# Performance work log

Hardware: AMD Instinct MI355X
Metric: run time of the kernel (lower is better)

Reference implementation:

```python
import jax
import jax.numpy as jnp
from jax import lax
import numpy as np

INPUT_DIM = 784
HIDDEN_DIM = 1024
BATCH = 256
N_BINS = 10


def setup_inputs() -> dict:
    key = jax.random.key(0)
    k1, k2, k3, k4, k5 = jax.random.split(key, 5)
    # kaiming-normal-ish init scales (faithful in spirit; exact values irrelevant for math)
    W = jax.random.normal(k1, (HIDDEN_DIM, INPUT_DIM), dtype=jnp.float32) * np.sqrt(2.0 / INPUT_DIM)
    c = jnp.zeros((HIDDEN_DIM, 1), dtype=jnp.float32)
    V = jax.random.normal(k2, (INPUT_DIM, HIDDEN_DIM, N_BINS), dtype=jnp.float32) * np.sqrt(2.0 / N_BINS)
    b = jnp.zeros((INPUT_DIM, N_BINS), dtype=jnp.float32)
    x = jax.random.randint(k3, (BATCH, INPUT_DIM), 0, N_BINS, dtype=jnp.int32)
    return {"x": x, "W": W, "c": c, "V": V, "b": b}


def reference(x, W, c, V, b):
    # x: [B, D] int pixel bins; W: [H, D]; c: [H, 1]; V: [D, H, 10]; b: [D, 10]
    B = x.shape[0]
    xf = x.astype(jnp.float32)  # [B, D]
    a0 = jnp.broadcast_to(c[:, 0][None, :], (B, W.shape[0]))  # [B, H]

    def step(a, inp):
        Vi, bi, Wi, xi = inp  # Vi:[H,10], bi:[10], Wi:[H], xi:[B]
        h = jax.nn.sigmoid(a)                       # [B, H]
        p = jax.nn.softmax(h @ Vi + bi, axis=1)     # [B, 10]
        a = a + xi[:, None] * Wi[None, :]           # rank-1 update, matches x_i @ W[:,i].T
        return a, p

    _, p_seq = lax.scan(step, a0, (V, b, W.T, xf.T))  # p_seq: [D, B, 10]
    p_hat = jnp.transpose(p_seq, (1, 2, 0))            # [B, 10, D] == torch.stack(p_hat, dim=2)
    return p_hat
```

## Files before the change

### kernel.cpp

```cpp
#include <hip/hip_runtime.h>
#include <stdint.h>

#define D_DIM 784
#define H_DIM 1024
#define B_DIM 256
#define NBIN  10
#define G_CH  16
#define T_CH  49
#define P_CH  8
#define T_PS  98
#define BT    16
#define LOG2E 1.4426950408889634f

#define VPREP_BLKS D_DIM
#define WPREP_BLKS 208

typedef _Float16 half8_t  __attribute__((ext_vector_type(8)));
typedef __fp16   fp16x2_t __attribute__((ext_vector_type(2)));
typedef float    float4_t __attribute__((ext_vector_type(4)));

__global__ void k_prep(const float* __restrict__ W, const float* __restrict__ V,
                       _Float16* __restrict__ Wt2h, _Float16* __restrict__ VB) {
    __shared__ __align__(16) float smem[5120];
    int tid = threadIdx.x;
    int bx  = blockIdx.x;

    if (bx < VPREP_BLKS) {
        int i = bx;
        const float4* src = (const float4*)(V + (size_t)i * H_DIM * NBIN);
        uint4* dst = (uint4*)VB + (size_t)i * 2048;
        #pragma unroll
        for (int p = 0; p < 2; ++p) {
            if (p) __syncthreads();
            #pragma unroll
            for (int qv = 0; qv < 5; ++qv) {
                float4 v = src[p * 1280 + qv * 256 + tid];
                *((float4*)&smem[(qv * 256 + tid) * 4]) = v;
            }
            __syncthreads();
            #pragma unroll
            for (int qv = 0; qv < 4; ++qv) {
                int pair = p * 1024 + qv * 256 + tid;
                int kk = pair >> 6, ll = pair & 63;
                int n = ll & 15, hb = kk * 32 + ((ll >> 4) & 3) * 8;
                union { _Float16 hh[8]; uint4 u; } o;
                #pragma unroll
                for (int jj = 0; jj < 8; ++jj)
                    o.hh[jj] = (_Float16)((n < NBIN) ? smem[(hb + jj) * NBIN + n - p * 5120] : 0.0f);
                dst[pair] = o.u;
            }
        }
    } else {
        int qw = bx - VPREP_BLKS;
        int j0 = (qw % 13) * 64, h0 = (qw / 13) * 64;
        float (*t)[65] = (float(*)[65])smem;
        int tj = tid & 63, tr = tid >> 6;
        int j = j0 + tj;
        #pragma unroll
        for (int r = 0; r < 16; ++r) {
            int hh = tr * 16 + r;
            t[hh][tj] = (j < D_DIM) ? W[(size_t)(h0 + hh) * D_DIM + j] : 0.0f;
        }
        __syncthreads();
        #pragma unroll
        for (int r = 0; r < 16; ++r) {
            int jj = tr * 16 + r;
            int jo = j0 + jj;
            if (jo < D_DIM) Wt2h[(size_t)jo * H_DIM + h0 + tj] = (_Float16)(t[tj][jj] * LOG2E);
        }
    }
}

__global__ __launch_bounds__(256)
void k_pscan(const _Float16* __restrict__ Wt2h, const int* __restrict__ x,
             const float* __restrict__ c, _Float16* __restrict__ PA) {
    int b   = blockIdx.x;
    int hg  = blockIdx.y;
    int tid = threadIdx.x;
    int hcol = hg * 256 + tid;
    int h0   = hcol * 2;

    __shared__ float xs[D_DIM];
    if (tid < D_DIM / 4) {
        int4 xi = ((const int4*)(x + (size_t)b * D_DIM))[tid];
        *((float4*)&xs[tid * 4]) =
            make_float4((float)xi.x, (float)xi.y, (float)xi.z, (float)xi.w);
    }
    float acc0 = c[h0] * LOG2E, acc1 = c[h0 + 1] * LOG2E;
    __syncthreads();

    const uint* wp  = (const uint*)Wt2h;
    uint*       pau = (uint*)PA;

    uint wvA[8], wvB[8];
    auto ldrow = [&](int t, uint (&wv)[8]) {
        #pragma unroll
        for (int r = 0; r < 8; ++r)
            wv[r] = wp[(size_t)(t * 8 + r) * 512 + hcol];
    };
    auto emit = [&](int t) {
        union { _Float16 hh[2]; uint u; } uu;
        uu.hh[0] = (_Float16)acc0; uu.hh[1] = (_Float16)acc1;
        pau[((size_t)t * B_DIM + b) * 512 + hcol] = uu.u;
    };
    auto fmas = [&](int t, const uint (&wv)[8]) {
        #pragma unroll
        for (int r = 0; r < 8; ++r) {
            union { uint u; _Float16 hh[2]; } uu; uu.u = wv[r];
            float xf = xs[t * 8 + r];
            acc0 += xf * (float)uu.hh[0];
            acc1 += xf * (float)uu.hh[1];
        }
    };

    ldrow(0, wvA);
    for (int t = 0; t < T_PS; t += 2) {
        ldrow(t + 1, wvB);
        emit(t);     fmas(t, wvA);
        if (t + 2 < T_PS) ldrow(t + 2, wvA);
        emit(t + 1); fmas(t + 1, wvB);
    }
}

__global__ __launch_bounds__(512, 2)
void k_main(const _Float16* __restrict__ VB, const _Float16* __restrict__ Wt2h,
            const _Float16* __restrict__ PA, const int* __restrict__ x,
            const float* __restrict__ bias, float* __restrict__ out) {
    int bid = blockIdx.x;
    int lb  = (bid & 7) * 98 + (bid >> 3);
    int tc  = lb >> 4;
    int bt  = lb & 15;
    int tid = threadIdx.x;
    int g   = tid >> 8;
    int w   = (tid >> 6) & 3;
    int l   = tid & 63;
    int bl  = l & 15;
    int kg  = l >> 4;
    int bg  = bt * BT + bl;
    int ib  = tc * G_CH;
    int i0  = ib + g * P_CH;

    __shared__ float red[2][4][64][17];
    __shared__ float bs[G_CH][16];

    {
        if (tid < 256) {
            int ii = tid >> 4, n = tid & 15;
            bs[ii][n] = (n < NBIN) ? bias[(size_t)(ib + ii) * NBIN + n] : 0.0f;
        }
    }

    float a[8][8];
    {
        int ct = tc * 2 + g;
        const _Float16* src = PA + ((size_t)ct * B_DIM + bg) * H_DIM + w * 256 + kg * 8;
        #pragma unroll
        for (int m = 0; m < 8; ++m) {
            half8_t av = *((const half8_t*)(src + m * 32));
            #pragma unroll
            for (int j = 0; j < 8; ++j) a[m][j] = (float)av[j];
        }
    }

    const int4* xp = (const int4*)(x + (size_t)bg * D_DIM + i0);

    const uint4* vp = (const uint4*)VB + ((size_t)i0 * 32 + w * 8) * 64 + l;
    uint4 vbuf[4];
    vbuf[0] = vp[0];
    vbuf[1] = vp[64];
    const uint4* vpr = vp + 128;

    const _Float16* whp = Wt2h + (size_t)i0 * H_DIM + w * 256 + kg * 8;
    half8_t whbuf[2];
    whbuf[0] = *((const half8_t*)whp);
    whbuf[1] = *((const half8_t*)(whp + 32));
    const _Float16* whr = whp + 64;

    float4_t acc = {0.f, 0.f, 0.f, 0.f};

    auto softmax_store = [&](int q) {
        float p4[4];
        #pragma unroll
        for (int qq = 0; qq < 4; ++qq) {
            float tot = red[g][0][l][qq * 4 + w] + red[g][1][l][qq * 4 + w]
                      + red[g][2][l][qq * 4 + w] + red[g][3][l][qq * 4 + w];
            float v = (bl < NBIN) ? tot + bs[g * P_CH + q * 4 + qq][bl] : -3.0e38f;
            float vm = v;
            vm = fmaxf(vm, __shfl_xor(vm, 1));
            vm = fmaxf(vm, __shfl_xor(vm, 2));
            vm = fmaxf(vm, __shfl_xor(vm, 4));
            vm = fmaxf(vm, __shfl_xor(vm, 8));
            float e = __builtin_amdgcn_exp2f((v - vm) * LOG2E);
            float ss = e;
            ss += __shfl_xor(ss, 1); ss += __shfl_xor(ss, 2);
            ss += __shfl_xor(ss, 4); ss += __shfl_xor(ss, 8);
            p4[qq] = e * __builtin_amdgcn_rcpf(ss);
        }
        if (bl < NBIN) {
            int b = bt * BT + kg * 4 + w;
            size_t base = ((size_t)b * NBIN + bl) * D_DIM + i0 + q * 4;
            *((float4*)(out + base)) = make_float4(p4[0], p4[1], p4[2], p4[3]);
        }
    };

    for (int q = 0; q < 2; ++q) {
        int4 xi = xp[q];
        float xq0 = (float)xi.x, xq1 = (float)xi.y, xq2 = (float)xi.z, xq3 = (float)xi.w;
        #pragma unroll
        for (int s = 0; s < 32; ++s) {
            const int iis = s >> 3;
            const int m   = s & 7;
            const int nn  = q * 32 + s + 2;
            half8_t wh = whbuf[s & 1];
            if (nn < 64) {
                vbuf[(s + 2) & 3] = *vpr;
                whbuf[s & 1] = *((const half8_t*)whr);
                vpr += (((s + 3) & 7) == 0) ? 1600 : 64;
                whr += (((s + 3) & 7) == 0) ? 800  : 32;
            }
            union { half8_t h8; uint u32[4]; } af;
            #pragma unroll
            for (int p = 0; p < 4; ++p) {
                float s0 = __builtin_amdgcn_rcpf(1.0f + __builtin_amdgcn_exp2f(-a[m][2 * p]));
                float s1 = __builtin_amdgcn_rcpf(1.0f + __builtin_amdgcn_exp2f(-a[m][2 * p + 1]));
                union { fp16x2_t v; uint u; } cv;
                cv.v = __builtin_amdgcn_cvt_pkrtz(s0, s1);
                af.u32[p] = cv.u;
            }
            union { half8_t h8; uint4 u; } bf;
            bf.u = vbuf[s & 3];
            acc = __builtin_amdgcn_mfma_f32_16x16x32_f16(af.h8, bf.h8, acc, 0, 0, 0);
            float xf = (iis == 0) ? xq0 : (iis == 1) ? xq1 : (iis == 2) ? xq2 : xq3;
            a[m][0] += xf * (float)wh[0]; a[m][1] += xf * (float)wh[1];
            a[m][2] += xf * (float)wh[2]; a[m][3] += xf * (float)wh[3];
            a[m][4] += xf * (float)wh[4]; a[m][5] += xf * (float)wh[5];
            a[m][6] += xf * (float)wh[6]; a[m][7] += xf * (float)wh[7];
            if (m == 7) {
                float* rp = &red[g][w][l][iis * 4];
                rp[0] = acc[0]; rp[1] = acc[1]; rp[2] = acc[2]; rp[3] = acc[3];
                acc = (float4_t){0.f, 0.f, 0.f, 0.f};
            }
        }
        __syncthreads();
        softmax_store(q);
        if (q == 0) __syncthreads();
    }
}

extern "C" void kernel_launch(void* const* d_in, const int* in_sizes, int n_in,
                              void* d_out, int out_size, void* d_ws, size_t ws_size,
                              hipStream_t stream) {
    const int*   x    = (const int*)d_in[0];
    const float* W    = (const float*)d_in[1];
    const float* c    = (const float*)d_in[2];
    const float* V    = (const float*)d_in[3];
    const float* bias = (const float*)d_in[4];
    float* out = (float*)d_out;

    char* ws = (char*)d_ws;
    size_t off = 0;
    _Float16* Wt2h = (_Float16*)(ws + off);
    off += (size_t)D_DIM * H_DIM * sizeof(_Float16);
    off = (off + 255) & ~(size_t)255;
    _Float16* VB = (_Float16*)(ws + off);
    off += (size_t)D_DIM * 32 * 64 * 8 * sizeof(_Float16);
    off = (off + 255) & ~(size_t)255;
    _Float16* PA = (_Float16*)(ws + off);

    k_prep<<<dim3(VPREP_BLKS + WPREP_BLKS), 256, 0, stream>>>(W, V, Wt2h, VB);
    k_pscan<<<dim3(B_DIM, 2), 256, 0, stream>>>(Wt2h, x, c, PA);
    k_main<<<dim3(D_DIM), 512, 0, stream>>>(VB, Wt2h, PA, x, bias, out);
}
```

Before: 200.6 us.

## Split k_main into 256-thread blocks per chunk and deepen pscan prefetch

k_main previously ran two 8-step chunk groups per 512-thread block. Now each 256-thread block handles a single 8-step chunk, with twice as many blocks and a new block-to-(tc,bt) mapping. The reduction buffer is indexed by q, which removes one __syncthreads per iteration. k_pscan now prefetches W rows four steps ahead instead of two, to hide more load latency at the cost of more registers.

```diff
diff --git a/kernel.cpp b/kernel.cpp
--- a/kernel.cpp
+++ b/kernel.cpp
@@ -5,8 +5,6 @@
 #define H_DIM 1024
 #define B_DIM 256
 #define NBIN  10
-#define G_CH  16
-#define T_CH  49
 #define P_CH  8
 #define T_PS  98
 #define BT    16
@@ -92,7 +90,7 @@
     const uint* wp  = (const uint*)Wt2h;
     uint*       pau = (uint*)PA;
 
-    uint wvA[8], wvB[8];
+    uint wv0[8], wv1[8], wv2[8], wv3[8];
     auto ldrow = [&](int t, uint (&wv)[8]) {
         #pragma unroll
         for (int r = 0; r < 8; ++r)
@@ -113,47 +111,53 @@
         }
     };
 
-    ldrow(0, wvA);
-    for (int t = 0; t < T_PS; t += 2) {
-        ldrow(t + 1, wvB);
-        emit(t);     fmas(t, wvA);
-        if (t + 2 < T_PS) ldrow(t + 2, wvA);
-        emit(t + 1); fmas(t + 1, wvB);
-    }
-}
-
-__global__ __launch_bounds__(512, 2)
+    ldrow(0, wv0); ldrow(1, wv1); ldrow(2, wv2); ldrow(3, wv3);
+    for (int t = 0; t < T_PS; t += 4) {
+        emit(t); fmas(t, wv0);
+        if (t + 4 < T_PS) ldrow(t + 4, wv0);
+        if (t + 1 < T_PS) {
+            emit(t + 1); fmas(t + 1, wv1);
+            if (t + 5 < T_PS) ldrow(t + 5, wv1);
+        }
+        if (t + 2 < T_PS) {
+            emit(t + 2); fmas(t + 2, wv2);
+            if (t + 6 < T_PS) ldrow(t + 6, wv2);
+        }
+        if (t + 3 < T_PS) {
+            emit(t + 3); fmas(t + 3, wv3);
+            if (t + 7 < T_PS) ldrow(t + 7, wv3);
+        }
+    }
+}
+
+__global__ __launch_bounds__(256, 4)
 void k_main(const _Float16* __restrict__ VB, const _Float16* __restrict__ Wt2h,
             const _Float16* __restrict__ PA, const int* __restrict__ x,
             const float* __restrict__ bias, float* __restrict__ out) {
     int bid = blockIdx.x;
-    int lb  = (bid & 7) * 98 + (bid >> 3);
-    int tc  = lb >> 4;
-    int bt  = lb & 15;
+    int bt  = ((bid & 7) << 1) | ((bid >> 3) & 1);
+    int tc  = bid >> 4;
     int tid = threadIdx.x;
-    int g   = tid >> 8;
-    int w   = (tid >> 6) & 3;
+    int w   = tid >> 6;
     int l   = tid & 63;
     int bl  = l & 15;
     int kg  = l >> 4;
     int bg  = bt * BT + bl;
-    int ib  = tc * G_CH;
-    int i0  = ib + g * P_CH;
+    int i0  = tc * P_CH;
 
     __shared__ float red[2][4][64][17];
-    __shared__ float bs[G_CH][16];
+    __shared__ float bs[P_CH][16];
 
     {
-        if (tid < 256) {
+        if (tid < P_CH * 16) {
             int ii = tid >> 4, n = tid & 15;
-            bs[ii][n] = (n < NBIN) ? bias[(size_t)(ib + ii) * NBIN + n] : 0.0f;
+            bs[ii][n] = (n < NBIN) ? bias[(size_t)(i0 + ii) * NBIN + n] : 0.0f;
         }
     }
 
     float a[8][8];
     {
-        int ct = tc * 2 + g;
-        const _Float16* src = PA + ((size_t)ct * B_DIM + bg) * H_DIM + w * 256 + kg * 8;
+        const _Float16* src = PA + ((size_t)tc * B_DIM + bg) * H_DIM + w * 256 + kg * 8;
         #pragma unroll
         for (int m = 0; m < 8; ++m) {
             half8_t av = *((const half8_t*)(src + m * 32));
@@ -182,9 +186,9 @@
         float p4[4];
         #pragma unroll
         for (int qq = 0; qq < 4; ++qq) {
-            float tot = red[g][0][l][qq * 4 + w] + red[g][1][l][qq * 4 + w]
-                      + red[g][2][l][qq * 4 + w] + red[g][3][l][qq * 4 + w];
-            float v = (bl < NBIN) ? tot + bs[g * P_CH + q * 4 + qq][bl] : -3.0e38f;
+            float tot = red[q][0][l][qq * 4 + w] + red[q][1][l][qq * 4 + w]
+                      + red[q][2][l][qq * 4 + w] + red[q][3][l][qq * 4 + w];
+            float v = (bl < NBIN) ? tot + bs[q * 4 + qq][bl] : -3.0e38f;
             float vm = v;
             vm = fmaxf(vm, __shfl_xor(vm, 1));
             vm = fmaxf(vm, __shfl_xor(vm, 2));
@@ -236,14 +240,13 @@
             a[m][4] += xf * (float)wh[4]; a[m][5] += xf * (float)wh[5];
             a[m][6] += xf * (float)wh[6]; a[m][7] += xf * (float)wh[7];
             if (m == 7) {
-                float* rp = &red[g][w][l][iis * 4];
+                float* rp = &red[q][w][l][iis * 4];
                 rp[0] = acc[0]; rp[1] = acc[1]; rp[2] = acc[2]; rp[3] = acc[3];
                 acc = (float4_t){0.f, 0.f, 0.f, 0.f};
             }
         }
         __syncthreads();
         softmax_store(q);
-        if (q == 0) __syncthreads();
     }
 }
 
@@ -269,5 +272,5 @@
 
     k_prep<<<dim3(VPREP_BLKS + WPREP_BLKS), 256, 0, stream>>>(W, V, Wt2h, VB);
     k_pscan<<<dim3(B_DIM, 2), 256, 0, stream>>>(Wt2h, x, c, PA);
-    k_main<<<dim3(D_DIM), 512, 0, stream>>>(VB, Wt2h, PA, x, bias, out);
-}
+    k_main<<<dim3(D_DIM * 2), 256, 0, stream>>>(VB, Wt2h, PA, x, bias, out);
+}
```

Measured after the change: 216.6 us. 7.9% more time.
